# Optimization experiments

Hardware: AMD Instinct MI355X
Metric: run time of the kernel (lower is better)

## Reference

```python
import jax, jax.numpy as jnp
import numpy as np

B, S, D_MODEL, N_HEADS, D_HEAD = 2, 2048, 2048, 16, 128


def _rope_tables(seq_len, d_head, base=10000.0):
    # standard llama RoPE cos/sin tables, broadcastable to (B, H, S, d_head)
    inv_freq = 1.0 / (base ** (np.arange(0, d_head, 2, dtype=np.float32) / d_head))
    t = np.arange(seq_len, dtype=np.float32)
    freqs = np.outer(t, inv_freq)                      # (S, d_head/2)
    emb = np.concatenate([freqs, freqs], axis=-1)       # (S, d_head)
    cos = jnp.asarray(np.cos(emb))[None, None]          # (1,1,S,d_head)
    sin = jnp.asarray(np.sin(emb))[None, None]
    return cos, sin


def setup_inputs() -> dict:
    key = jax.random.key(0)
    ks = jax.random.split(key, 5)
    scale = 0.02
    x = jax.random.normal(ks[0], (B, S, D_MODEL), dtype=jnp.float32)
    Wq = jax.random.normal(ks[1], (D_MODEL, D_MODEL), dtype=jnp.float32) * scale
    Wk = jax.random.normal(ks[2], (D_MODEL, D_MODEL), dtype=jnp.float32) * scale
    Wv = jax.random.normal(ks[3], (D_MODEL, D_MODEL), dtype=jnp.float32) * scale
    Wo = jax.random.normal(ks[4], (D_MODEL, D_MODEL), dtype=jnp.float32) * scale
    cos, sin = _rope_tables(S, D_HEAD)
    return {"x": x, "cos": cos, "sin": sin, "Wq": Wq, "Wk": Wk, "Wv": Wv, "Wo": Wo}


def _rotate_half(x):
    x1, x2 = jnp.split(x, 2, axis=-1)
    return jnp.concatenate([-x2, x1], axis=-1)


def _apply_rope(x, cos, sin):
    return x * cos + _rotate_half(x) * sin


def reference(x, cos, sin, Wq, Wk, Wv, Wo):
    b, s, _ = x.shape
    # QKV projections (nn.Linear computes x @ W.T), reshape to (B, H, S, Dh)
    def proj(W):
        return (x @ W.T).reshape(b, s, N_HEADS, D_HEAD).transpose(0, 2, 1, 3)
    q = _apply_rope(proj(Wq), cos, sin)
    k = _apply_rope(proj(Wk), cos, sin)
    v = proj(Wv)
    # causal scaled dot-product attention
    scale = 1.0 / jnp.sqrt(jnp.asarray(D_HEAD, dtype=x.dtype))
    scores = jnp.einsum("bhqd,bhkd->bhqk", q, k) * scale
    causal = jnp.tril(jnp.ones((s, s), dtype=bool))
    scores = jnp.where(causal, scores, jnp.asarray(-jnp.inf, dtype=scores.dtype))
    attn = jax.nn.softmax(scores, axis=-1)
    vals = jnp.einsum("bhqk,bhkd->bhqd", attn, v)
    vals = vals.transpose(0, 2, 1, 3).reshape(b, s, D_MODEL)
    return vals @ Wo.T
```

## Files before the change

### kernel.cpp

```cpp
#include <hip/hip_runtime.h>

#define S_LEN 2048
#define DMODEL 2048
#define NHEADS 16
#define DHEAD 128
#define BATCH 2

typedef unsigned short u16;
typedef __attribute__((ext_vector_type(8))) __bf16 bf16x8;
typedef __attribute__((ext_vector_type(4))) float f32x4;

__device__ __forceinline__ u16 f2bf(float f) {
    union { float f; unsigned int u; } a; a.f = f;
    unsigned int u = a.u;
    u += 0x7fffu + ((u >> 16) & 1u);
    return (u16)(u >> 16);
}
__device__ __forceinline__ u16 f2bf_fast(float f) {
    union { float f; unsigned int u; } a; a.f = f;
    return (u16)((a.u + 0x8000u) >> 16);
}
__device__ __forceinline__ float bf2f(u16 b) {
    union { unsigned int u; float f; } a; a.u = ((unsigned int)b) << 16;
    return a.f;
}

__device__ __forceinline__ void g2l16(const void* g, void* l) {
    __builtin_amdgcn_global_load_lds((const __attribute__((address_space(1))) unsigned int*)g,
                                     (__attribute__((address_space(3))) unsigned int*)l,
                                     16, 0, 0);
}

__global__ void cvt_all(const float* __restrict__ x,
                        const float* __restrict__ w0, const float* __restrict__ w1,
                        const float* __restrict__ w2, const float* __restrict__ w3,
                        u16* __restrict__ xb, u16* __restrict__ wdst) {
    int y = blockIdx.y;
    const float* src;
    u16* out;
    if (y < 2) {
        src = x + (size_t)y * 4194304;
        out = xb + (size_t)y * 4194304;
    } else {
        src = (y == 2) ? w0 : (y == 3) ? w1 : (y == 4) ? w2 : w3;
        out = wdst + (size_t)(y - 2) * DMODEL * DMODEL;
    }
    int i = blockIdx.x * 256 + threadIdx.x;
    f32x4 v = *(const f32x4*)(src + (size_t)i * 4);
    ushort4 o;
    o.x = f2bf(v[0]); o.y = f2bf(v[1]); o.z = f2bf(v[2]); o.w = f2bf(v[3]);
    *(ushort4*)(out + (size_t)i * 4) = o;
}

#define QK_PRESCALE 0.12751744f
__global__ void rope_kernel(u16* __restrict__ Q, u16* __restrict__ K,
                            const float* __restrict__ cosT, const float* __restrict__ sinT) {
    u16* T = blockIdx.z ? K : Q;
    const float pre = blockIdx.z ? 1.0f : QK_PRESCALE;
    int bh = blockIdx.y;
    int t = blockIdx.x * 256 + threadIdx.x;
    int s = t >> 4;
    int d4 = (t & 15) * 4;
    u16* row = T + ((size_t)bh * S_LEN + s) * DHEAD;
    ushort4 lo = *(ushort4*)&row[d4];
    ushort4 hi = *(ushort4*)&row[d4 + 64];
    f32x4 cv = *(const f32x4*)&cosT[s * DHEAD + d4];
    f32x4 sv = *(const f32x4*)&sinT[s * DHEAD + d4];
    float l0 = bf2f(lo.x), l1 = bf2f(lo.y), l2 = bf2f(lo.z), l3 = bf2f(lo.w);
    float h0 = bf2f(hi.x), h1 = bf2f(hi.y), h2 = bf2f(hi.z), h3 = bf2f(hi.w);
    ushort4 olo, ohi;
    olo.x = f2bf((l0 * cv[0] - h0 * sv[0]) * pre);
    olo.y = f2bf((l1 * cv[1] - h1 * sv[1]) * pre);
    olo.z = f2bf((l2 * cv[2] - h2 * sv[2]) * pre);
    olo.w = f2bf((l3 * cv[3] - h3 * sv[3]) * pre);
    ohi.x = f2bf((h0 * cv[0] + l0 * sv[0]) * pre);
    ohi.y = f2bf((h1 * cv[1] + l1 * sv[1]) * pre);
    ohi.z = f2bf((h2 * cv[2] + l2 * sv[2]) * pre);
    ohi.w = f2bf((h3 * cv[3] + l3 * sv[3]) * pre);
    *(ushort4*)&row[d4]      = olo;
    *(ushort4*)&row[d4 + 64] = ohi;
}

__global__ __launch_bounds__(256) void gemm_qkv(const u16* __restrict__ A,
                                                const u16* __restrict__ W,
                                                u16* __restrict__ Qo,
                                                u16* __restrict__ Ko,
                                                u16* __restrict__ Vto) {
    __shared__ u16 As[128 * 32];
    __shared__ u16 Ws[128 * 32];
    const int tid  = threadIdx.x;
    const int lane = tid & 63;
    const int wave = tid >> 6;
    const int wm = wave >> 1, wn = wave & 1;
    const int col = lane & 15, quad = lane >> 4;
    const int blk = blockIdx.x;
    const int xcd = blk & 7;
    const int loc = blk >> 3;
    const int nb  = xcd * 6 + loc % 6;
    const int mb  = loc / 6;
    const int m0 = mb * 128, n0 = nb * 128;
    const int K = DMODEL;
    const int which = n0 >> 11;

    const u16* P0 = (which == 2) ? A : W;
    const u16* P1 = (which == 2) ? W : A;
    const int  r0 = (which == 2) ? m0 : n0;
    const int  r1 = (which == 2) ? n0 : m0;

    f32x4 acc[4][4] = {};

    const int swl = (quad ^ ((col >> 1) & 3)) * 8;
    int a_off[4], w_off[4];
    #pragma unroll
    for (int mi = 0; mi < 4; ++mi) a_off[mi] = (wm * 64 + mi * 16 + col) * 32 + swl;
    #pragma unroll
    for (int ni = 0; ni < 4; ++ni) w_off[ni] = (wn * 64 + ni * 16 + col) * 32 + swl;

    for (int kk = 0; kk < K; kk += 32) {
        #pragma unroll
        for (int i = 0; i < 2; ++i) {
            int c = i * 256 + tid;
            int row = c >> 2;
            int ko = (((c & 3) ^ ((c >> 3) & 3))) * 8;
            int cb = i * 256 + wave * 64;
            g2l16(P0 + (size_t)(r0 + row) * K + kk + ko, (void*)(As + cb * 8));
            g2l16(P1 + (size_t)(r1 + row) * K + kk + ko, (void*)(Ws + cb * 8));
        }
        __syncthreads();
        bf16x8 af[4], wf[4];
        #pragma unroll
        for (int mi = 0; mi < 4; ++mi) af[mi] = *(const bf16x8*)&As[a_off[mi]];
        #pragma unroll
        for (int ni = 0; ni < 4; ++ni) wf[ni] = *(const bf16x8*)&Ws[w_off[ni]];
        #pragma unroll
        for (int mi = 0; mi < 4; ++mi)
            #pragma unroll
            for (int ni = 0; ni < 4; ++ni)
                acc[mi][ni] = __builtin_amdgcn_mfma_f32_16x16x32_bf16(af[mi], wf[ni], acc[mi][ni], 0, 0, 0);
        __syncthreads();
    }

    if (which == 2) {
        #pragma unroll
        for (int mi = 0; mi < 4; ++mi) {
            #pragma unroll
            for (int ni = 0; ni < 4; ++ni) {
                int s0   = m0 + wm * 64 + mi * 16 + quad * 4;
                int ncol = (n0 & 2047) + wn * 64 + ni * 16 + col;
                int b = s0 >> 11, s = s0 & 2047;
                int h = ncol >> 7, d = ncol & 127;
                ushort4 o;
                o.x = f2bf(acc[mi][ni][0]); o.y = f2bf(acc[mi][ni][1]);
                o.z = f2bf(acc[mi][ni][2]); o.w = f2bf(acc[mi][ni][3]);
                *(ushort4*)&Vto[(((size_t)(b * NHEADS + h)) * DHEAD + d) * S_LEN + s] = o;
            }
        }
    } else {
        u16* out = which ? Ko : Qo;
        #pragma unroll
        for (int mi = 0; mi < 4; ++mi) {
            #pragma unroll
            for (int ni = 0; ni < 4; ++ni) {
                int dd = (n0 & 2047) + wm * 64 + mi * 16 + quad * 4;
                int sg = m0 + wn * 64 + ni * 16 + col;
                int b = sg >> 11, s = sg & 2047;
                int h = dd >> 7, d = dd & 127;
                ushort4 o;
                o.x = f2bf(acc[mi][ni][0]); o.y = f2bf(acc[mi][ni][1]);
                o.z = f2bf(acc[mi][ni][2]); o.w = f2bf(acc[mi][ni][3]);
                *(ushort4*)&out[(((size_t)(b * NHEADS + h)) * S_LEN + s) * DHEAD + d] = o;
            }
        }
    }
}

__global__ __launch_bounds__(256) void gemm_out(const u16* __restrict__ A,
                                                const u16* __restrict__ W,
                                                float* __restrict__ out) {
    __shared__ u16 As[128 * 32];
    __shared__ u16 Ws[128 * 32];
    const int tid  = threadIdx.x;
    const int lane = tid & 63;
    const int wave = tid >> 6;
    const int wm = wave >> 1, wn = wave & 1;
    const int col = lane & 15, quad = lane >> 4;
    const int blk = blockIdx.x;
    const int xcd = blk & 7;
    const int loc = blk >> 3;
    const int nb  = xcd * 2 + (loc & 1);
    const int mb  = loc >> 1;
    const int m0 = mb * 128, n0 = nb * 128;
    const int K = DMODEL;

    f32x4 acc[4][4] = {};

    const int swl = (quad ^ ((col >> 1) & 3)) * 8;
    int a_off[4], w_off[4];
    #pragma unroll
    for (int mi = 0; mi < 4; ++mi) a_off[mi] = (wm * 64 + mi * 16 + col) * 32 + swl;
    #pragma unroll
    for (int ni = 0; ni < 4; ++ni) w_off[ni] = (wn * 64 + ni * 16 + col) * 32 + swl;

    for (int kk = 0; kk < K; kk += 32) {
        #pragma unroll
        for (int i = 0; i < 2; ++i) {
            int c = i * 256 + tid;
            int row = c >> 2;
            int ko = (((c & 3) ^ ((c >> 3) & 3))) * 8;
            int cb = i * 256 + wave * 64;
            g2l16(A + (size_t)(m0 + row) * K + kk + ko, (void*)(As + cb * 8));
            g2l16(W + (size_t)(n0 + row) * K + kk + ko, (void*)(Ws + cb * 8));
        }
        __syncthreads();
        bf16x8 af[4], wf[4];
        #pragma unroll
        for (int mi = 0; mi < 4; ++mi) af[mi] = *(const bf16x8*)&As[a_off[mi]];
        #pragma unroll
        for (int ni = 0; ni < 4; ++ni) wf[ni] = *(const bf16x8*)&Ws[w_off[ni]];
        #pragma unroll
        for (int mi = 0; mi < 4; ++mi)
            #pragma unroll
            for (int ni = 0; ni < 4; ++ni)
                acc[mi][ni] = __builtin_amdgcn_mfma_f32_16x16x32_bf16(af[mi], wf[ni], acc[mi][ni], 0, 0, 0);
        __syncthreads();
    }

    #pragma unroll
    for (int mi = 0; mi < 4; ++mi)
        #pragma unroll
        for (int ni = 0; ni < 4; ++ni)
            #pragma unroll
            for (int r = 0; r < 4; ++r) {
                int row  = m0 + wm * 64 + mi * 16 + quad * 4 + r;
                int ncol = n0 + wn * 64 + ni * 16 + col;
                out[(size_t)row * DMODEL + ncol] = acc[mi][ni][r];
            }
}

__global__ __launch_bounds__(256) void attn_kernel(const u16* __restrict__ Q,
                                                   const u16* __restrict__ K,
                                                   const u16* __restrict__ Vt,
                                                   u16* __restrict__ Ao) {
    __shared__ u16 Ks[64 * 136];
    __shared__ u16 Vs[128 * 72];
    __shared__ u16 Ps[4][16 * 40];

    const int tid  = threadIdx.x;
    const int lane = tid & 63;
    const int wave = tid >> 6;
    const int col = lane & 15, quad = lane >> 4;
    const int xcd = blockIdx.x & 7;
    const int sub = (blockIdx.x >> 3) & 3;
    const int bh  = xcd * 4 + sub;
    const int qtile = 31 - (int)(blockIdx.x >> 5);
    const int b = bh >> 4, h = bh & 15;
    const int qb = qtile * 64;
    const int qw = qb + wave * 16;

    const u16* Qb = Q  + (size_t)bh * S_LEN * DHEAD;
    const u16* Kb = K  + (size_t)bh * S_LEN * DHEAD;
    const u16* Vb = Vt + (size_t)bh * DHEAD * S_LEN;

    bf16x8 qf[4];
    #pragma unroll
    for (int dc = 0; dc < 4; ++dc)
        qf[dc] = *(const bf16x8*)&Qb[(size_t)(qw + col) * DHEAD + dc * 32 + quad * 8];

    f32x4 accO[8] = {};
    float lrow = 0.0f;

    int krr[4], koo[4], vrr[4], voo[4];
    #pragma unroll
    for (int i = 0; i < 4; ++i) {
        int vid = i * 256 + tid;
        krr[i] = vid >> 4; koo[i] = (vid & 15) * 8;
        vrr[i] = vid >> 3; voo[i] = (vid & 7) * 8;
    }

    f32x4 kv[4], vv[4];
    #pragma unroll
    for (int i = 0; i < 4; ++i) {
        kv[i] = *(const f32x4*)&Kb[(size_t)krr[i] * DHEAD + koo[i]];
        vv[i] = *(const f32x4*)&Vb[(size_t)vrr[i] * S_LEN + voo[i]];
    }

    const int kend = qb + 64;
    for (int kb = 0; kb < kend; kb += 64) {
        #pragma unroll
        for (int i = 0; i < 4; ++i) {
            *(f32x4*)&Ks[krr[i] * 136 + koo[i]] = kv[i];
            *(f32x4*)&Vs[vrr[i] * 72 + voo[i]] = vv[i];
        }
        __syncthreads();

        const int kn = kb + 64;
        if (kn < kend) {
            #pragma unroll
            for (int i = 0; i < 4; ++i) {
                kv[i] = *(const f32x4*)&Kb[(size_t)(kn + krr[i]) * DHEAD + koo[i]];
                vv[i] = *(const f32x4*)&Vb[(size_t)vrr[i] * S_LEN + kn + voo[i]];
            }
        }

        #pragma unroll
        for (int sb = 0; sb < 2; ++sb) {
            const int kbs = kb + sb * 32;
            if (kbs <= qw + 15) {
                f32x4 sc[2] = {};
                #pragma unroll
                for (int t = 0; t < 2; ++t)
                    #pragma unroll
                    for (int dc = 0; dc < 4; ++dc) {
                        bf16x8 kf = *(const bf16x8*)&Ks[(sb * 32 + t * 16 + col) * 136 + dc * 32 + quad * 8];
                        sc[t] = __builtin_amdgcn_mfma_f32_16x16x32_bf16(kf, qf[dc], sc[t], 0, 0, 0);
                    }

                const int q_g = qw + col;
                float p[2][4];
                #pragma unroll
                for (int t = 0; t < 2; ++t)
                    #pragma unroll
                    for (int r = 0; r < 4; ++r) {
                        int k_g = kbs + t * 16 + quad * 4 + r;
                        float e = exp2f(sc[t][r]);
                        p[t][r] = (k_g <= q_g) ? e : 0.0f;
                        lrow += p[t][r];
                    }

                u16* P = Ps[wave];
                #pragma unroll
                for (int t = 0; t < 2; ++t) {
                    ushort4 o;
                    o.x = f2bf_fast(p[t][0]); o.y = f2bf_fast(p[t][1]);
                    o.z = f2bf_fast(p[t][2]); o.w = f2bf_fast(p[t][3]);
                    *(ushort4*)&P[col * 40 + t * 16 + quad * 4] = o;
                }
                asm volatile("s_waitcnt lgkmcnt(0)" ::: "memory");
                bf16x8 pf = *(const bf16x8*)&P[col * 40 + quad * 8];

                #pragma unroll
                for (int ni = 0; ni < 8; ++ni) {
                    bf16x8 vf = *(const bf16x8*)&Vs[(ni * 16 + col) * 72 + sb * 32 + quad * 8];
                    accO[ni] = __builtin_amdgcn_mfma_f32_16x16x32_bf16(pf, vf, accO[ni], 0, 0, 0);
                }
            }
        }
        __syncthreads();
    }

    lrow += __shfl_xor(lrow, 16);
    lrow += __shfl_xor(lrow, 32);
    float lb[4];
    #pragma unroll
    for (int r = 0; r < 4; ++r)
        lb[r] = 1.0f / __shfl(lrow, quad * 4 + r);
    #pragma unroll
    for (int ni = 0; ni < 8; ++ni)
        #pragma unroll
        for (int r = 0; r < 4; ++r) {
            int q_g = qw + quad * 4 + r;
            int d = ni * 16 + col;
            Ao[((size_t)(b * S_LEN + q_g)) * DMODEL + h * DHEAD + d] = f2bf(accO[ni][r] * lb[r]);
        }
}

extern "C" void kernel_launch(void* const* d_in, const int* in_sizes, int n_in,
                              void* d_out, int out_size, void* d_ws, size_t ws_size,
                              hipStream_t stream) {
    const float* x    = (const float*)d_in[0];
    const float* cosT = (const float*)d_in[1];
    const float* sinT = (const float*)d_in[2];
    const float* Wq   = (const float*)d_in[3];
    const float* Wk   = (const float*)d_in[4];
    const float* Wv   = (const float*)d_in[5];
    const float* Wo   = (const float*)d_in[6];

    char* ws = (char*)d_ws;
    size_t off = 0;
    auto carve = [&](size_t bytes) {
        void* p = ws + off;
        off += (bytes + 255) & ~(size_t)255;
        return p;
    };
    const size_t xN = (size_t)BATCH * S_LEN * DMODEL;
    const size_t wN = (size_t)DMODEL * DMODEL;
    u16* xb   = (u16*)carve(xN * 2);
    u16* wqkv = (u16*)carve(wN * 2 * 4);
    u16* wob  = wqkv + wN * 3;
    u16* Qb   = (u16*)carve(xN * 2);
    u16* Kb   = (u16*)carve(xN * 2);
    u16* Vtb  = (u16*)carve(xN * 2);
    u16* attn = xb;

    cvt_all<<<dim3(4096, 6), 256, 0, stream>>>(x, Wq, Wk, Wv, Wo, xb, wqkv);

    gemm_qkv<<<dim3(1536), 256, 0, stream>>>(xb, wqkv, Qb, Kb, Vtb);

    rope_kernel<<<dim3(S_LEN * 16 / 256, BATCH * NHEADS, 2), 256, 0, stream>>>(Qb, Kb, cosT, sinT);

    attn_kernel<<<dim3(1024), 256, 0, stream>>>(Qb, Kb, Vtb, attn);

    gemm_out<<<dim3(512), 256, 0, stream>>>(attn, wob, (float*)d_out);
}
```

Before: 388.6 us.

## Rewrite QKV GEMM with 256x256 tiles and double-buffered async LDS pipeline

The fused QKV projection GEMM moves from 128x128 tiles with 256 threads and a synchronous load-then-compute K loop to 256x256 tiles with 512 threads. It stages K=64 slices into double-buffered swizzled LDS, issuing the loads in quarter-stages interleaved with the MFMA phases and ordering them with explicit waitcnt, barriers and setprio. The goal is more operand reuse per block and hiding global-load latency behind matrix math. In exchange it needs 128 KB of LDS per block, fewer blocks (384), and fragile hand-written synchronisation.

Result: slower. 433.4 us (+11.5%).

```diff
diff --git a/kernel.cpp b/kernel.cpp
--- a/kernel.cpp
+++ b/kernel.cpp
@@ -81,96 +81,140 @@
     *(ushort4*)&row[d4 + 64] = ohi;
 }
 
-__global__ __launch_bounds__(256) void gemm_qkv(const u16* __restrict__ A,
-                                                const u16* __restrict__ W,
-                                                u16* __restrict__ Qo,
-                                                u16* __restrict__ Ko,
-                                                u16* __restrict__ Vto) {
-    __shared__ u16 As[128 * 32];
-    __shared__ u16 Ws[128 * 32];
-    const int tid  = threadIdx.x;
-    const int lane = tid & 63;
-    const int wave = tid >> 6;
-    const int wm = wave >> 1, wn = wave & 1;
+
+template<int KIND>
+__device__ __forceinline__ void stage_u(const u16* __restrict__ src, int r0,
+                                        u16 (*Lh)[8192], int kt, int tid) {
+    const int row  = tid >> 3;
+    const int wrow = row & ~7;
+    const int csw  = ((tid & 7) ^ (row & 7)) * 8;
+    int rowm, rowmW;
+    if (KIND == 0)      { rowm = row;                   rowmW = wrow; }
+    else if (KIND == 2) { rowm = row + 64;              rowmW = wrow + 64; }
+    else if (KIND == 1) { rowm = row + (row & 32);      rowmW = wrow + (wrow & 32); }
+    else                { rowm = row + 32 + (row & 32); rowmW = wrow + 32 + (wrow & 32); }
+    #pragma unroll
+    for (int j = 0; j < 2; ++j)
+        g2l16(src + (size_t)(r0 + j * 128 + rowm) * DMODEL + kt + csw,
+              (void*)(Lh[j] + rowmW * 64));
+}
+
+__global__ __launch_bounds__(512, 2) void gemm_qkv(const u16* __restrict__ A,
+                                                   const u16* __restrict__ W,
+                                                   u16* __restrict__ Qo,
+                                                   u16* __restrict__ Ko,
+                                                   u16* __restrict__ Vto) {
+    __shared__ u16 LA[2][2][8192];
+    __shared__ u16 LB[2][2][8192];
+
+    const int tid = threadIdx.x, lane = tid & 63, wave = tid >> 6;
+    const int wm = wave >> 2, wn = wave & 3;
     const int col = lane & 15, quad = lane >> 4;
-    const int blk = blockIdx.x;
-    const int xcd = blk & 7;
-    const int loc = blk >> 3;
-    const int nb  = xcd * 6 + loc % 6;
-    const int mb  = loc / 6;
-    const int m0 = mb * 128, n0 = nb * 128;
-    const int K = DMODEL;
-    const int which = n0 >> 11;
-
-    const u16* P0 = (which == 2) ? A : W;
-    const u16* P1 = (which == 2) ? W : A;
-    const int  r0 = (which == 2) ? m0 : n0;
-    const int  r1 = (which == 2) ? n0 : m0;
-
-    f32x4 acc[4][4] = {};
-
-    const int swl = (quad ^ ((col >> 1) & 3)) * 8;
-    int a_off[4], w_off[4];
-    #pragma unroll
-    for (int mi = 0; mi < 4; ++mi) a_off[mi] = (wm * 64 + mi * 16 + col) * 32 + swl;
-    #pragma unroll
-    for (int ni = 0; ni < 4; ++ni) w_off[ni] = (wn * 64 + ni * 16 + col) * 32 + swl;
-
-    for (int kk = 0; kk < K; kk += 32) {
-        #pragma unroll
-        for (int i = 0; i < 2; ++i) {
-            int c = i * 256 + tid;
-            int row = c >> 2;
-            int ko = (((c & 3) ^ ((c >> 3) & 3))) * 8;
-            int cb = i * 256 + wave * 64;
-            g2l16(P0 + (size_t)(r0 + row) * K + kk + ko, (void*)(As + cb * 8));
-            g2l16(P1 + (size_t)(r1 + row) * K + kk + ko, (void*)(Ws + cb * 8));
-        }
-        __syncthreads();
-        bf16x8 af[4], wf[4];
-        #pragma unroll
-        for (int mi = 0; mi < 4; ++mi) af[mi] = *(const bf16x8*)&As[a_off[mi]];
-        #pragma unroll
-        for (int ni = 0; ni < 4; ++ni) wf[ni] = *(const bf16x8*)&Ws[w_off[ni]];
-        #pragma unroll
-        for (int mi = 0; mi < 4; ++mi)
-            #pragma unroll
-            for (int ni = 0; ni < 4; ++ni)
-                acc[mi][ni] = __builtin_amdgcn_mfma_f32_16x16x32_bf16(af[mi], wf[ni], acc[mi][ni], 0, 0, 0);
-        __syncthreads();
-    }
-
-    if (which == 2) {
-        #pragma unroll
-        for (int mi = 0; mi < 4; ++mi) {
+    const int orig = blockIdx.x;
+    const int blk = (orig & 7) * 48 + (orig >> 3);
+    const int region = blk >> 7;
+    const int local  = blk & 127;
+
+    const u16* Aop; const u16* Bop; int r0a, r0b;
+    if (region < 2) {
+        Aop = W; r0a = region * 2048 + (local & 7) * 256;
+        Bop = A; r0b = (local >> 3) * 256;
+    } else {
+        Aop = A; r0a = (local >> 3) * 256;
+        Bop = W; r0b = 4096 + (local & 7) * 256;
+    }
+
+    f32x4 acc[8][4] = {};
+    const int swz0 = (quad ^ (col & 7)) * 8;
+    const int swz1 = ((4 + quad) ^ (col & 7)) * 8;
+    const int rB = (wn & 1) * 64;
+
+    stage_u<0>(Aop, r0a, LA[0], 0, tid);
+    stage_u<1>(Bop, r0b, LB[0], 0, tid);
+    stage_u<2>(Aop, r0a, LA[0], 0, tid);
+    stage_u<3>(Bop, r0b, LB[0], 0, tid);
+    stage_u<0>(Aop, r0a, LA[1], 64, tid);
+    stage_u<1>(Bop, r0b, LB[1], 64, tid);
+
+    for (int t = 0; t < 32; ++t) {
+        const int bsel = t & 1, nb = bsel ^ 1;
+        const int kt1 = (t + 1) * 64, kt2 = (t + 2) * 64;
+        const u16* Ah = LA[bsel][wm];
+        const u16* Bh = LB[bsel][wn >> 1];
+        #pragma unroll
+        for (int p = 0; p < 4; ++p) {
+            const int mi0 = (p >> 1) * 4, ni0 = (p & 1) * 2;
+            bf16x8 af[4][2], bfr[2][2];
+            if (p == 0) {
+                if (t < 31) {
+                    asm volatile("s_waitcnt vmcnt(4)" ::: "memory");
+                    stage_u<2>(Aop, r0a, LA[nb], kt1, tid);
+                } else {
+                    asm volatile("s_waitcnt vmcnt(0)" ::: "memory");
+                }
+                __builtin_amdgcn_s_barrier();
+            }
+            #pragma unroll
+            for (int i = 0; i < 4; ++i) {
+                int r = (mi0 + i) * 16 + col;
+                af[i][0] = *(const bf16x8*)&Ah[r * 64 + swz0];
+                af[i][1] = *(const bf16x8*)&Ah[r * 64 + swz1];
+            }
+            #pragma unroll
+            for (int j = 0; j < 2; ++j) {
+                int r = rB + (ni0 + j) * 16 + col;
+                bfr[j][0] = *(const bf16x8*)&Bh[r * 64 + swz0];
+                bfr[j][1] = *(const bf16x8*)&Bh[r * 64 + swz1];
+            }
+            if (p == 1)      { if (t < 31) stage_u<3>(Bop, r0b, LB[nb], kt1, tid); }
+            else if (p == 2) { if (t < 30) stage_u<0>(Aop, r0a, LA[bsel], kt2, tid); }
+            else if (p == 3) { if (t < 30) stage_u<1>(Bop, r0b, LB[bsel], kt2, tid); }
+            if (p != 0) __builtin_amdgcn_s_barrier();
+            asm volatile("s_waitcnt lgkmcnt(0)" ::: "memory");
+            __builtin_amdgcn_sched_barrier(0);
+            __builtin_amdgcn_s_setprio(1);
+            #pragma unroll
+            for (int ks = 0; ks < 2; ++ks)
+                #pragma unroll
+                for (int i = 0; i < 4; ++i)
+                    #pragma unroll
+                    for (int j = 0; j < 2; ++j)
+                        acc[mi0 + i][ni0 + j] = __builtin_amdgcn_mfma_f32_16x16x32_bf16(
+                            af[i][ks], bfr[j][ks], acc[mi0 + i][ni0 + j], 0, 0, 0);
+            __builtin_amdgcn_s_setprio(0);
+            __builtin_amdgcn_s_barrier();
+        }
+    }
+
+    if (region < 2) {
+        u16* out = region ? Ko : Qo;
+        #pragma unroll
+        for (int mi = 0; mi < 8; ++mi)
             #pragma unroll
             for (int ni = 0; ni < 4; ++ni) {
-                int s0   = m0 + wm * 64 + mi * 16 + quad * 4;
-                int ncol = (n0 & 2047) + wn * 64 + ni * 16 + col;
-                int b = s0 >> 11, s = s0 & 2047;
-                int h = ncol >> 7, d = ncol & 127;
+                int d_g = r0a + wm * 128 + mi * 16 + quad * 4;
+                int s_g = r0b + wn * 64 + ni * 16 + col;
+                int b = s_g >> 11, s = s_g & 2047;
+                int h = (d_g >> 7) & 15, d = d_g & 127;
+                ushort4 o;
+                o.x = f2bf(acc[mi][ni][0]); o.y = f2bf(acc[mi][ni][1]);
+                o.z = f2bf(acc[mi][ni][2]); o.w = f2bf(acc[mi][ni][3]);
+                *(ushort4*)&out[(((size_t)(b * NHEADS + h)) * S_LEN + s) * DHEAD + d] = o;
+            }
+    } else {
+        #pragma unroll
+        for (int mi = 0; mi < 8; ++mi)
+            #pragma unroll
+            for (int ni = 0; ni < 4; ++ni) {
+                int s_g = r0a + wm * 128 + mi * 16 + quad * 4;
+                int d_g = (r0b - 4096) + wn * 64 + ni * 16 + col;
+                int b = s_g >> 11, s = s_g & 2047;
+                int h = d_g >> 7, d = d_g & 127;
                 ushort4 o;
                 o.x = f2bf(acc[mi][ni][0]); o.y = f2bf(acc[mi][ni][1]);
                 o.z = f2bf(acc[mi][ni][2]); o.w = f2bf(acc[mi][ni][3]);
                 *(ushort4*)&Vto[(((size_t)(b * NHEADS + h)) * DHEAD + d) * S_LEN + s] = o;
             }
-        }
-    } else {
-        u16* out = which ? Ko : Qo;
-        #pragma unroll
-        for (int mi = 0; mi < 4; ++mi) {
-            #pragma unroll
-            for (int ni = 0; ni < 4; ++ni) {
-                int dd = (n0 & 2047) + wm * 64 + mi * 16 + quad * 4;
-                int sg = m0 + wn * 64 + ni * 16 + col;
-                int b = sg >> 11, s = sg & 2047;
-                int h = dd >> 7, d = dd & 127;
-                ushort4 o;
-                o.x = f2bf(acc[mi][ni][0]); o.y = f2bf(acc[mi][ni][1]);
-                o.z = f2bf(acc[mi][ni][2]); o.w = f2bf(acc[mi][ni][3]);
-                *(ushort4*)&out[(((size_t)(b * NHEADS + h)) * S_LEN + s) * DHEAD + d] = o;
-            }
-        }
     }
 }
 
@@ -394,7 +438,7 @@
 
     cvt_all<<<dim3(4096, 6), 256, 0, stream>>>(x, Wq, Wk, Wv, Wo, xb, wqkv);
 
-    gemm_qkv<<<dim3(1536), 256, 0, stream>>>(xb, wqkv, Qb, Kb, Vtb);
+    gemm_qkv<<<dim3(384), 512, 0, stream>>>(xb, wqkv, Qb, Kb, Vtb);
 
     rope_kernel<<<dim3(S_LEN * 16 / 256, BATCH * NHEADS, 2), 256, 0, stream>>>(Qb, Kb, cosT, sinT);
 
```
